# Kernel optimization log

Hardware: AMD Instinct MI355X
Metric: run time of the kernel (lower is better)

The kernel has to match this reference:

```python
import jax, jax.numpy as jnp
import numpy as np

D_MODEL = 1024
NUM_HEADS = 16
DEPTH = D_MODEL // NUM_HEADS
NEG_INF_SCALE = -1e9


def setup_inputs() -> dict:
    key = jax.random.key(0)
    ks = jax.random.split(key, 12)
    B, S = 2, 2048
    q = jax.random.normal(ks[0], (B, S, D_MODEL), dtype=jnp.float32)
    k = jax.random.normal(ks[1], (B, S, D_MODEL), dtype=jnp.float32)
    v = jax.random.normal(ks[2], (B, S, D_MODEL), dtype=jnp.float32)
    # causal mask: 1 where attention is disallowed (future positions)
    mask = jnp.triu(jnp.ones((S, S), dtype=jnp.float32), k=1)[None, None]
    scale = 1.0 / np.sqrt(D_MODEL)
    Wq = jax.random.normal(ks[3], (D_MODEL, D_MODEL), dtype=jnp.float32) * scale
    bq = jnp.zeros((D_MODEL,), dtype=jnp.float32)
    Wk = jax.random.normal(ks[4], (D_MODEL, D_MODEL), dtype=jnp.float32) * scale
    bk = jnp.zeros((D_MODEL,), dtype=jnp.float32)
    Wv = jax.random.normal(ks[5], (D_MODEL, D_MODEL), dtype=jnp.float32) * scale
    bv = jnp.zeros((D_MODEL,), dtype=jnp.float32)
    Wo = jax.random.normal(ks[6], (D_MODEL, D_MODEL), dtype=jnp.float32) * scale
    bo = jnp.zeros((D_MODEL,), dtype=jnp.float32)
    return {"v": v, "k": k, "q": q, "mask": mask,
            "Wq": Wq, "bq": bq, "Wk": Wk, "bk": bk,
            "Wv": Wv, "bv": bv, "Wo": Wo, "bo": bo}


def _split_heads(x):
    B, S, _ = x.shape
    return x.reshape(B, S, NUM_HEADS, DEPTH).transpose(0, 2, 1, 3)  # [B,H,S,depth]


def reference(v, k, q, mask, Wq, bq, Wk, bk, Wv, bv, Wo, bo):
    B, Sq, _ = q.shape
    qh = _split_heads(q @ Wq + bq)  # [B,H,Sq,depth]
    kh = _split_heads(k @ Wk + bk)  # [B,H,Sk,depth]
    vh = _split_heads(v @ Wv + bv)  # [B,H,Sk,depth]
    logits = jnp.einsum('bhqd,bhkd->bhqk', qh, kh) / jnp.sqrt(
        jnp.asarray(DEPTH, dtype=jnp.float32))
    logits = logits + mask * NEG_INF_SCALE
    attn = jax.nn.softmax(logits, axis=-1)
    out = jnp.einsum('bhqk,bhkd->bhqd', attn, vh)  # [B,H,Sq,depth]
    out = out.transpose(0, 2, 1, 3).reshape(B, Sq, D_MODEL)
    return out @ Wo + bo
```

## Files before the change

kernel.cpp:

```cpp
#include <hip/hip_runtime.h>
#include <stdint.h>

#define D_MODEL 1024
#define NHEADS  16
#define DEPTH   64
#define BATCH   2
#define SEQ     2048
#define M_TOT   (BATCH * SEQ)

#define Q_SCALE 0.18033688011112042f

typedef unsigned short u16;
typedef unsigned int   u32;
typedef __attribute__((ext_vector_type(8))) short bf16x8;
typedef __attribute__((ext_vector_type(4))) float f32x4;

__device__ __forceinline__ float bf2f(unsigned int u) {
    union { unsigned int i; float f; } x;
    x.i = (u & 0xffffu) << 16;
    return x.f;
}
__device__ __forceinline__ u16 f2bf(float f) {
    union { float f; unsigned int i; } x;
    x.f = f;
    unsigned int lsb = (x.i >> 16) & 1u;
    x.i += 0x7fffu + lsb;
    return (u16)(x.i >> 16);
}
__device__ __forceinline__ u32 fbits(float f) {
    union { float f; unsigned int i; } x; x.f = f; return x.i;
}
__device__ __forceinline__ float exp2f_hw(float x) {
    return __builtin_amdgcn_exp2f(x);
}

__device__ __forceinline__ int sniff_f32(const u16* q) {
    const int lane = threadIdx.x & 63;
    int cnt = 0;
    #pragma unroll
    for (int j = 0; j < 4; ++j) {
        unsigned int bits = q[2 * (lane + 64 * j)];
        bool susp = ((bits & 0x7fffu) >= 0x4780u);
        cnt += (int)__popcll(__ballot(susp));
    }
    return (cnt >= 32) ? 1 : 0;
}

template <int CTRL>
__device__ __forceinline__ float dppf(float x) {
    int r = __builtin_amdgcn_update_dpp(0, (int)fbits(x), CTRL, 0xF, 0xF, false);
    union { int i; float f; } u; u.i = r; return u.f;
}
__device__ __forceinline__ float redmax16(float x) {
    x = fmaxf(x, dppf<0xB1>(x));
    x = fmaxf(x, dppf<0x4E>(x));
    x = fmaxf(x, dppf<0x124>(x));
    x = fmaxf(x, dppf<0x128>(x));
    return x;
}
__device__ __forceinline__ float redsum16(float x) {
    x += dppf<0xB1>(x);
    x += dppf<0x4E>(x);
    x += dppf<0x124>(x);
    x += dppf<0x128>(x);
    return x;
}

__device__ __forceinline__ void stage16(const u16* g, u16* ldsbase) {
#if __has_builtin(__builtin_amdgcn_global_load_lds)
    __builtin_amdgcn_global_load_lds(
        (const __attribute__((address_space(1))) unsigned int*)g,
        (__attribute__((address_space(3))) unsigned int*)ldsbase, 16, 0, 0);
#else
    int lane = threadIdx.x & 63;
    *(uint4*)(ldsbase + lane * 8) = *(const uint4*)g;
#endif
}

__global__ __launch_bounds__(256)
void prep_kernel(const void* q, const void* k, const void* v,
                 const void* W0, const void* W1, const void* W2, const void* W3,
                 u16* d0, u16* d1, u16* d2,
                 u16* T0, u16* T1, u16* T2, u16* T3) {
    __shared__ u16 t[64][72];
    const int f32 = sniff_f32((const u16*)q);
    const int tid = threadIdx.x;
    const int bid = blockIdx.x;

    if (bid < 6144) {
        const int z = bid / 2048, bx = bid % 2048;
        const void* src = (z == 0) ? q : (z == 1) ? k : v;
        u16* dst = (z == 0) ? d0 : (z == 1) ? d1 : d2;
        const size_t i = ((size_t)bx * 256 + tid) * 8;
        if (f32) {
            const float* s = (const float*)src + i;
            float4 a = *(const float4*)s;
            float4 b = *(const float4*)(s + 4);
            u16 t8[8];
            t8[0] = f2bf(a.x); t8[1] = f2bf(a.y); t8[2] = f2bf(a.z); t8[3] = f2bf(a.w);
            t8[4] = f2bf(b.x); t8[5] = f2bf(b.y); t8[6] = f2bf(b.z); t8[7] = f2bf(b.w);
            *(uint4*)(dst + i) = *(uint4*)t8;
        } else {
            *(uint4*)(dst + i) = *(const uint4*)((const u16*)src + i);
        }
    } else {
        const int r = bid - 6144;
        const int z = r >> 8, rem = r & 255;
        const int n0 = (rem & 15) * 64, k0 = (rem >> 4) * 64;
        const void* Wv = (z == 0) ? W0 : (z == 1) ? W1 : (z == 2) ? W2 : W3;
        u16* WT = (z == 0) ? T0 : (z == 1) ? T1 : (z == 2) ? T2 : T3;

        #pragma unroll
        for (int cb = 0; cb < 2; ++cb) {
            int c = tid + cb * 256;
            int kl = c >> 3, nc = (c & 7) * 8;
            size_t off = (size_t)(k0 + kl) * D_MODEL + n0 + nc;
            u16 tmp[8];
            if (f32) {
                const float* W = (const float*)Wv;
                float4 a = *(const float4*)(W + off);
                float4 b = *(const float4*)(W + off + 4);
                tmp[0] = f2bf(a.x); tmp[1] = f2bf(a.y); tmp[2] = f2bf(a.z); tmp[3] = f2bf(a.w);
                tmp[4] = f2bf(b.x); tmp[5] = f2bf(b.y); tmp[6] = f2bf(b.z); tmp[7] = f2bf(b.w);
            } else {
                *(uint4*)tmp = *(const uint4*)((const u16*)Wv + off);
            }
            *(uint4*)&t[kl][nc] = *(uint4*)tmp;
        }
        __syncthreads();
        #pragma unroll
        for (int cb = 0; cb < 2; ++cb) {
            int c = tid + cb * 256;
            int nl = c >> 3, kc = (c & 7) * 8;
            u16 tmp[8];
            #pragma unroll
            for (int i = 0; i < 8; ++i) tmp[i] = t[kc + i][nl];
            *(uint4*)(WT + (size_t)(n0 + nl) * D_MODEL + k0 + kc) = *(uint4*)tmp;
        }
    }
}

struct GemmJob {
    const u16*  A;
    const u16*  BT;
    const void* bias;
    void*       C;
    int cmode;
    float scale;
};

__global__ __launch_bounds__(256, 4)
void gemm6(GemmJob j0, GemmJob j1, GemmJob j2, const u16* __restrict__ qs) {
    __shared__ u16 Als[2][64 * 64];
    __shared__ u16 Bls[2][64 * 64];

    const u32 lin = blockIdx.x + gridDim.x * (blockIdx.y + gridDim.y * blockIdx.z);
    const u32 xcd = lin & 7, idx = lin >> 3;
    const u32 per = (gridDim.y * gridDim.z) >> 3;
    const u32 mz = xcd * per + (idx >> 3);
    const u32 nb_ = idx & 7;
    const u32 zz = mz / gridDim.y;
    const u32 my2 = mz % gridDim.y;
    const u32 mtile = my2 >> 1, nhalf = my2 & 1;
    GemmJob jb = (zz == 0) ? j0 : (zz == 1) ? j1 : j2;

    const int f32 = sniff_f32(qs);
    const int tid = threadIdx.x;
    const int w = tid >> 6, lane = tid & 63;
    const int cc = lane & 15, quad = lane >> 4;
    const int wm = w >> 1, wn = w & 1;
    const int m0 = mtile * 64, n0 = (nhalf * 8 + nb_) * 64;

    f32x4 zero4 = {0.f, 0.f, 0.f, 0.f};
    f32x4 acc[2][2];
    #pragma unroll
    for (int i = 0; i < 2; ++i)
        #pragma unroll
        for (int j = 0; j < 2; ++j) acc[i][j] = zero4;

    const int srow_off = lane >> 3;
    const int sg8 = ((lane & 7) ^ ((lane >> 3) & 7)) * 8;

    auto stageAB = [&](int buf, int k0) {
        #pragma unroll
        for (int i = 0; i < 2; ++i) {
            int c = w * 2 + i;
            int row = c * 8 + srow_off;
            stage16(jb.BT + (size_t)(n0 + row) * D_MODEL + k0 + sg8, &Bls[buf][c * 512]);
            stage16(jb.A  + (size_t)(m0 + row) * D_MODEL + k0 + sg8, &Als[buf][c * 512]);
        }
    };

    stageAB(0, 0);

    const int NT = D_MODEL / 64;
    for (int t = 0; t < NT; ++t) {
        const int cur = t & 1;
        __syncthreads();
        if (t + 1 < NT) stageAB(cur ^ 1, (t + 1) * 64);

        const int sw = cc & 7;
        bf16x8 af[2][2], bf[2][2];
        #pragma unroll
        for (int i = 0; i < 2; ++i) {
            const u16* ar = &Als[cur][(wm * 32 + i * 16 + cc) * 64];
            af[i][0] = *(const bf16x8*)(ar + ((quad ^ sw) * 8));
            af[i][1] = *(const bf16x8*)(ar + (((4 + quad) ^ sw) * 8));
        }
        #pragma unroll
        for (int j = 0; j < 2; ++j) {
            const u16* br = &Bls[cur][(wn * 32 + j * 16 + cc) * 64];
            bf[j][0] = *(const bf16x8*)(br + ((quad ^ sw) * 8));
            bf[j][1] = *(const bf16x8*)(br + (((4 + quad) ^ sw) * 8));
        }
        __builtin_amdgcn_s_setprio(1);
        #pragma unroll
        for (int i = 0; i < 2; ++i)
            #pragma unroll
            for (int j = 0; j < 2; ++j) {
                acc[i][j] = __builtin_amdgcn_mfma_f32_16x16x32_bf16(af[i][0], bf[j][0], acc[i][j], 0, 0, 0);
                acc[i][j] = __builtin_amdgcn_mfma_f32_16x16x32_bf16(af[i][1], bf[j][1], acc[i][j], 0, 0, 0);
            }
        __builtin_amdgcn_s_setprio(0);
    }

    #pragma unroll
    for (int j = 0; j < 2; ++j) {
        int col = n0 + wn * 32 + j * 16 + cc;
        float bv = f32 ? ((const float*)jb.bias)[col] : bf2f(((const u16*)jb.bias)[col]);
        #pragma unroll
        for (int i = 0; i < 2; ++i)
            #pragma unroll
            for (int r = 0; r < 4; ++r) {
                int row = m0 + wm * 32 + i * 16 + quad * 4 + r;
                float vo = (acc[i][j][r] + bv) * jb.scale;
                if (jb.cmode == 0) {
                    ((u16*)jb.C)[(size_t)row * D_MODEL + col] = f2bf(vo);
                } else if (jb.cmode == 1) {
                    int bb = row >> 11, tok = row & (SEQ - 1);
                    int hh = col >> 6, dd = col & 63;
                    int tile = tok >> 6, n = tok & 63;
                    int kap = ((n & 15) << 2) + (n >> 4);
                    ((u16*)jb.C)[((size_t)((bb * NHEADS + hh) * DEPTH + dd)) * SEQ
                                 + tile * 64 + kap] = f2bf(vo);
                } else {
                    if (f32) ((float*)jb.C)[(size_t)row * D_MODEL + col] = vo;
                    else     ((u16*)jb.C)[(size_t)row * D_MODEL + col] = f2bf(vo);
                }
            }
    }
}

__global__ __launch_bounds__(256, 3)
void attn3(const u16* __restrict__ Qp, const u16* __restrict__ Kp,
           const u16* __restrict__ VpT, u16* __restrict__ Ao) {
    __shared__ u16 Kls[2][64 * 64];
    __shared__ u16 Vls[2][64 * 64];
    __shared__ u16 Pls[4][16][72];

    const int tid = threadIdx.x;
    const int w = tid >> 6, lane = tid & 63;
    const int cc = lane & 15, quad = lane >> 4;

    const u32 lin = blockIdx.x + 32u * (blockIdx.y + 16u * blockIdx.z);
    const int qq = 31 - (int)(lin >> 5);
    const int h  = (int)(lin & 15);
    const int b  = (int)((lin >> 4) & 1);
    const int qbase = qq * 64 + w * 16;

    bf16x8 qf[2];
    {
        const u16* qr = Qp + (size_t)(b * SEQ + qbase + cc) * D_MODEL + h * DEPTH;
        qf[0] = *(const bf16x8*)(qr + quad * 8);
        qf[1] = *(const bf16x8*)(qr + 32 + quad * 8);
    }

    const u16* kbase = Kp + (size_t)(b * SEQ) * D_MODEL + h * DEPTH;
    const u16* vbase = VpT + (size_t)((b * NHEADS + h) * DEPTH) * SEQ;

    const int r8 = lane >> 3;
    const int g8 = ((lane & 7) ^ (r8 & 7)) * 8;

    auto stageKV = [&](int buf, int jt) {
        #pragma unroll
        for (int i = 0; i < 2; ++i) {
            int row = w * 16 + i * 8 + r8;
            stage16(kbase + (size_t)(jt * 64 + row) * D_MODEL + g8,
                    &Kls[buf][(w * 16 + i * 8) * 64]);
            stage16(vbase + (size_t)row * SEQ + jt * 64 + g8,
                    &Vls[buf][(w * 16 + i * 8) * 64]);
        }
    };

    f32x4 zero4 = {0.f, 0.f, 0.f, 0.f};
    f32x4 oacc[4];
    #pragma unroll
    for (int db = 0; db < 4; ++db) oacc[db] = zero4;
    float m_run[4], l_run[4];
    #pragma unroll
    for (int r = 0; r < 4; ++r) { m_run[r] = -1e30f; l_run[r] = 0.f; }

    stageKV(0, 0);

    for (int jt = 0; jt <= qq; ++jt) {
        const int cur = jt & 1;
        __syncthreads();
        if (jt < qq) stageKV(cur ^ 1, jt + 1);

        const int sw = cc & 7;
        bf16x8 kf[4][2];
        #pragma unroll
        for (int nb = 0; nb < 4; ++nb) {
            const u16* kr = &Kls[cur][(nb * 16 + cc) * 64];
            kf[nb][0] = *(const bf16x8*)(kr + ((quad ^ sw) * 8));
            kf[nb][1] = *(const bf16x8*)(kr + (((4 + quad) ^ sw) * 8));
        }
        f32x4 s[4];
        __builtin_amdgcn_s_setprio(1);
        #pragma unroll
        for (int nb = 0; nb < 4; ++nb) {
            s[nb] = __builtin_amdgcn_mfma_f32_16x16x32_bf16(qf[0], kf[nb][0], zero4, 0, 0, 0);
            s[nb] = __builtin_amdgcn_mfma_f32_16x16x32_bf16(qf[1], kf[nb][1], s[nb], 0, 0, 0);
        }
        __builtin_amdgcn_s_setprio(0);

        if (jt == qq) {
            #pragma unroll
            for (int nb = 0; nb < 4; ++nb)
                #pragma unroll
                for (int r = 0; r < 4; ++r)
                    if (nb * 16 + cc > w * 16 + quad * 4 + r) s[nb][r] = -1e30f;
        }

        float alpha[4];
        #pragma unroll
        for (int r = 0; r < 4; ++r) {
            float mrow = redmax16(fmaxf(fmaxf(s[0][r], s[1][r]),
                                        fmaxf(s[2][r], s[3][r])));
            float mn = fmaxf(m_run[r], mrow);
            alpha[r] = exp2f_hw(m_run[r] - mn);
            m_run[r] = mn;
        }
        #pragma unroll
        for (int nb = 0; nb < 4; ++nb)
            #pragma unroll
            for (int r = 0; r < 4; ++r)
                s[nb][r] = exp2f_hw(s[nb][r] - m_run[r]);
        #pragma unroll
        for (int r = 0; r < 4; ++r)
            l_run[r] = l_run[r] * alpha[r]
                     + ((s[0][r] + s[1][r]) + (s[2][r] + s[3][r]));
        #pragma unroll
        for (int db = 0; db < 4; ++db)
            #pragma unroll
            for (int r = 0; r < 4; ++r)
                oacc[db][r] *= alpha[r];

        #pragma unroll
        for (int r = 0; r < 4; ++r) {
            u32 p01 = __builtin_amdgcn_perm(fbits(s[1][r]), fbits(s[0][r]), 0x07060302u);
            u32 p23 = __builtin_amdgcn_perm(fbits(s[3][r]), fbits(s[2][r]), 0x07060302u);
            uint2 pk; pk.x = p01; pk.y = p23;
            *(uint2*)&Pls[w][quad * 4 + r][4 * cc] = pk;
        }
        __asm__ volatile("" ::: "memory");

        bf16x8 pf0 = *(const bf16x8*)&Pls[w][cc][quad * 8];
        bf16x8 pf1 = *(const bf16x8*)&Pls[w][cc][32 + quad * 8];

        __builtin_amdgcn_s_setprio(1);
        #pragma unroll
        for (int db = 0; db < 4; ++db) {
            const u16* vr = &Vls[cur][(db * 16 + cc) * 64];
            bf16x8 v0 = *(const bf16x8*)(vr + ((quad ^ sw) * 8));
            bf16x8 v1 = *(const bf16x8*)(vr + (((4 + quad) ^ sw) * 8));
            oacc[db] = __builtin_amdgcn_mfma_f32_16x16x32_bf16(pf0, v0, oacc[db], 0, 0, 0);
            oacc[db] = __builtin_amdgcn_mfma_f32_16x16x32_bf16(pf1, v1, oacc[db], 0, 0, 0);
        }
        __builtin_amdgcn_s_setprio(0);
    }

    float linv[4];
    #pragma unroll
    for (int r = 0; r < 4; ++r) linv[r] = 1.0f / redsum16(l_run[r]);
    #pragma unroll
    for (int db = 0; db < 4; ++db)
        #pragma unroll
        for (int r = 0; r < 4; ++r) {
            size_t row = (size_t)(b * SEQ + qbase + quad * 4 + r);
            Ao[row * D_MODEL + h * DEPTH + db * 16 + cc] =
                f2bf(oacc[db][r] * linv[r]);
        }
}

extern "C" void kernel_launch(void* const* d_in, const int* in_sizes, int n_in,
                              void* d_out, int out_size, void* d_ws, size_t ws_size,
                              hipStream_t stream) {
    const void* v  = d_in[0];
    const void* k  = d_in[1];
    const void* q  = d_in[2];
    const void* Wq = d_in[4];
    const void* bq = d_in[5];
    const void* Wk = d_in[6];
    const void* bk = d_in[7];
    const void* Wv = d_in[8];
    const void* bv = d_in[9];
    const void* Wo = d_in[10];
    const void* bo = d_in[11];

    char* base = (char*)d_ws;
    const size_t WSZ = (size_t)D_MODEL * D_MODEL;
    const size_t TOK = (size_t)M_TOT * D_MODEL;
    u16* WqT = (u16*)(base + 256);
    u16* WkT = WqT + WSZ;
    u16* WvT = WkT + WSZ;
    u16* WoT = WvT + WSZ;
    u16* Qb  = WoT + WSZ;
    u16* Kb  = Qb + TOK;
    u16* Vb  = Kb + TOK;
    u16* Qp  = Vb + TOK;
    u16* Kp  = Qp + TOK;
    u16* VpT = Kp + TOK;
    u16* Ao  = Qb;

    prep_kernel<<<dim3(7168), 256, 0, stream>>>(q, k, v, Wq, Wk, Wv, Wo,
                                                Qb, Kb, Vb,
                                                WqT, WkT, WvT, WoT);

    GemmJob jq = {Qb, WqT, bq, Qp,    0, Q_SCALE};
    GemmJob jk = {Kb, WkT, bk, Kp,    0, 1.0f};
    GemmJob jv = {Vb, WvT, bv, VpT,   1, 1.0f};
    gemm6<<<dim3(8, 128, 3), 256, 0, stream>>>(jq, jk, jv, (const u16*)q);

    attn3<<<dim3(32, 16, 2), 256, 0, stream>>>(Qp, Kp, VpT, Ao);

    GemmJob jo = {Ao, WoT, bo, d_out, 2, 1.0f};
    gemm6<<<dim3(8, 128, 1), 256, 0, stream>>>(jo, jo, jo, (const u16*)q);
}
```

Before: 244.8 us.

## Fuse fp32-to-bf16 activation conversion into QKV projection GEMM A-tile loads

Drops the separate prep pass that converts q, k and v from fp32 to bf16 buffers. The projection GEMM now loads fp32 A tiles into registers, converts them and writes them to LDS after the MFMAs, while B still uses the direct global-to-LDS path. This removes a full read and write of the activations, but each GEMM block reads twice as many A bytes and does the conversion inside the main loop, which adds register pressure.

```diff
diff --git a/kernel.cpp b/kernel.cpp
--- a/kernel.cpp
+++ b/kernel.cpp
@@ -78,74 +78,54 @@
 }
 
 __global__ __launch_bounds__(256)
-void prep_kernel(const void* q, const void* k, const void* v,
+void prep_kernel(const u16* q,
                  const void* W0, const void* W1, const void* W2, const void* W3,
-                 u16* d0, u16* d1, u16* d2,
                  u16* T0, u16* T1, u16* T2, u16* T3) {
     __shared__ u16 t[64][72];
-    const int f32 = sniff_f32((const u16*)q);
+    const int f32 = sniff_f32(q);
     const int tid = threadIdx.x;
-    const int bid = blockIdx.x;
-
-    if (bid < 6144) {
-        const int z = bid / 2048, bx = bid % 2048;
-        const void* src = (z == 0) ? q : (z == 1) ? k : v;
-        u16* dst = (z == 0) ? d0 : (z == 1) ? d1 : d2;
-        const size_t i = ((size_t)bx * 256 + tid) * 8;
+    const int r = blockIdx.x;
+    const int z = r >> 8, rem = r & 255;
+    const int n0 = (rem & 15) * 64, k0 = (rem >> 4) * 64;
+    const void* Wv = (z == 0) ? W0 : (z == 1) ? W1 : (z == 2) ? W2 : W3;
+    u16* WT = (z == 0) ? T0 : (z == 1) ? T1 : (z == 2) ? T2 : T3;
+
+    #pragma unroll
+    for (int cb = 0; cb < 2; ++cb) {
+        int c = tid + cb * 256;
+        int kl = c >> 3, nc = (c & 7) * 8;
+        size_t off = (size_t)(k0 + kl) * D_MODEL + n0 + nc;
+        u16 tmp[8];
         if (f32) {
-            const float* s = (const float*)src + i;
-            float4 a = *(const float4*)s;
-            float4 b = *(const float4*)(s + 4);
-            u16 t8[8];
-            t8[0] = f2bf(a.x); t8[1] = f2bf(a.y); t8[2] = f2bf(a.z); t8[3] = f2bf(a.w);
-            t8[4] = f2bf(b.x); t8[5] = f2bf(b.y); t8[6] = f2bf(b.z); t8[7] = f2bf(b.w);
-            *(uint4*)(dst + i) = *(uint4*)t8;
+            const float* W = (const float*)Wv;
+            float4 a = *(const float4*)(W + off);
+            float4 b = *(const float4*)(W + off + 4);
+            tmp[0] = f2bf(a.x); tmp[1] = f2bf(a.y); tmp[2] = f2bf(a.z); tmp[3] = f2bf(a.w);
+            tmp[4] = f2bf(b.x); tmp[5] = f2bf(b.y); tmp[6] = f2bf(b.z); tmp[7] = f2bf(b.w);
         } else {
-            *(uint4*)(dst + i) = *(const uint4*)((const u16*)src + i);
-        }
-    } else {
-        const int r = bid - 6144;
-        const int z = r >> 8, rem = r & 255;
-        const int n0 = (rem & 15) * 64, k0 = (rem >> 4) * 64;
-        const void* Wv = (z == 0) ? W0 : (z == 1) ? W1 : (z == 2) ? W2 : W3;
-        u16* WT = (z == 0) ? T0 : (z == 1) ? T1 : (z == 2) ? T2 : T3;
-
-        #pragma unroll
-        for (int cb = 0; cb < 2; ++cb) {
-            int c = tid + cb * 256;
-            int kl = c >> 3, nc = (c & 7) * 8;
-            size_t off = (size_t)(k0 + kl) * D_MODEL + n0 + nc;
-            u16 tmp[8];
-            if (f32) {
-                const float* W = (const float*)Wv;
-                float4 a = *(const float4*)(W + off);
-                float4 b = *(const float4*)(W + off + 4);
-                tmp[0] = f2bf(a.x); tmp[1] = f2bf(a.y); tmp[2] = f2bf(a.z); tmp[3] = f2bf(a.w);
-                tmp[4] = f2bf(b.x); tmp[5] = f2bf(b.y); tmp[6] = f2bf(b.z); tmp[7] = f2bf(b.w);
-            } else {
-                *(uint4*)tmp = *(const uint4*)((const u16*)Wv + off);
-            }
-            *(uint4*)&t[kl][nc] = *(uint4*)tmp;
-        }
-        __syncthreads();
-        #pragma unroll
-        for (int cb = 0; cb < 2; ++cb) {
-            int c = tid + cb * 256;
-            int nl = c >> 3, kc = (c & 7) * 8;
-            u16 tmp[8];
-            #pragma unroll
-            for (int i = 0; i < 8; ++i) tmp[i] = t[kc + i][nl];
-            *(uint4*)(WT + (size_t)(n0 + nl) * D_MODEL + k0 + kc) = *(uint4*)tmp;
-        }
+            *(uint4*)tmp = *(const uint4*)((const u16*)Wv + off);
+        }
+        *(uint4*)&t[kl][nc] = *(uint4*)tmp;
+    }
+    __syncthreads();
+    #pragma unroll
+    for (int cb = 0; cb < 2; ++cb) {
+        int c = tid + cb * 256;
+        int nl = c >> 3, kc = (c & 7) * 8;
+        u16 tmp[8];
+        #pragma unroll
+        for (int i = 0; i < 8; ++i) tmp[i] = t[kc + i][nl];
+        *(uint4*)(WT + (size_t)(n0 + nl) * D_MODEL + k0 + kc) = *(uint4*)tmp;
     }
 }
 
 struct GemmJob {
-    const u16*  A;
+    const void* A;
     const u16*  BT;
     const void* bias;
     void*       C;
     int cmode;
+    int araw;
     float scale;
 };
 
@@ -180,24 +160,62 @@
 
     const int srow_off = lane >> 3;
     const int sg8 = ((lane & 7) ^ ((lane >> 3) & 7)) * 8;
-
-    auto stageAB = [&](int buf, int k0) {
+    const bool acvt = jb.araw && f32;
+
+    auto stageB = [&](int buf, int k0) {
         #pragma unroll
         for (int i = 0; i < 2; ++i) {
             int c = w * 2 + i;
             int row = c * 8 + srow_off;
             stage16(jb.BT + (size_t)(n0 + row) * D_MODEL + k0 + sg8, &Bls[buf][c * 512]);
-            stage16(jb.A  + (size_t)(m0 + row) * D_MODEL + k0 + sg8, &Als[buf][c * 512]);
         }
     };
-
-    stageAB(0, 0);
+    auto stageA_bf = [&](int buf, int k0) {
+        #pragma unroll
+        for (int i = 0; i < 2; ++i) {
+            int c = w * 2 + i;
+            int row = c * 8 + srow_off;
+            stage16((const u16*)jb.A + (size_t)(m0 + row) * D_MODEL + k0 + sg8,
+                    &Als[buf][c * 512]);
+        }
+    };
+    float4 a0v[2], a1v[2];
+    auto aload_f32 = [&](int k0) {
+        #pragma unroll
+        for (int i = 0; i < 2; ++i) {
+            int c = w * 2 + i;
+            int row = c * 8 + srow_off;
+            const float* s = (const float*)jb.A + (size_t)(m0 + row) * D_MODEL + k0 + sg8;
+            a0v[i] = *(const float4*)s;
+            a1v[i] = *(const float4*)(s + 4);
+        }
+    };
+    auto awrite_f32 = [&](int buf) {
+        #pragma unroll
+        for (int i = 0; i < 2; ++i) {
+            int c = w * 2 + i;
+            u16 t8[8];
+            t8[0] = f2bf(a0v[i].x); t8[1] = f2bf(a0v[i].y);
+            t8[2] = f2bf(a0v[i].z); t8[3] = f2bf(a0v[i].w);
+            t8[4] = f2bf(a1v[i].x); t8[5] = f2bf(a1v[i].y);
+            t8[6] = f2bf(a1v[i].z); t8[7] = f2bf(a1v[i].w);
+            *(uint4*)&Als[buf][c * 512 + lane * 8] = *(uint4*)t8;
+        }
+    };
+
+    if (acvt) { aload_f32(0); stageB(0, 0); awrite_f32(0); }
+    else      { stageA_bf(0, 0); stageB(0, 0); }
 
     const int NT = D_MODEL / 64;
     for (int t = 0; t < NT; ++t) {
         const int cur = t & 1;
         __syncthreads();
-        if (t + 1 < NT) stageAB(cur ^ 1, (t + 1) * 64);
+        const bool pf = (t + 1 < NT);
+        if (pf) {
+            stageB(cur ^ 1, (t + 1) * 64);
+            if (acvt) aload_f32((t + 1) * 64);
+            else      stageA_bf(cur ^ 1, (t + 1) * 64);
+        }
 
         const int sw = cc & 7;
         bf16x8 af[2][2], bf[2][2];
@@ -222,6 +240,8 @@
                 acc[i][j] = __builtin_amdgcn_mfma_f32_16x16x32_bf16(af[i][1], bf[j][1], acc[i][j], 0, 0, 0);
             }
         __builtin_amdgcn_s_setprio(0);
+
+        if (pf && acvt) awrite_f32(cur ^ 1);
     }
 
     #pragma unroll
@@ -415,25 +435,21 @@
     u16* WkT = WqT + WSZ;
     u16* WvT = WkT + WSZ;
     u16* WoT = WvT + WSZ;
-    u16* Qb  = WoT + WSZ;
-    u16* Kb  = Qb + TOK;
-    u16* Vb  = Kb + TOK;
-    u16* Qp  = Vb + TOK;
+    u16* Qp  = WoT + WSZ;
     u16* Kp  = Qp + TOK;
     u16* VpT = Kp + TOK;
-    u16* Ao  = Qb;
-
-    prep_kernel<<<dim3(7168), 256, 0, stream>>>(q, k, v, Wq, Wk, Wv, Wo,
-                                                Qb, Kb, Vb,
+    u16* Ao  = VpT + TOK;
+
+    prep_kernel<<<dim3(1024), 256, 0, stream>>>((const u16*)q, Wq, Wk, Wv, Wo,
                                                 WqT, WkT, WvT, WoT);
 
-    GemmJob jq = {Qb, WqT, bq, Qp,    0, Q_SCALE};
-    GemmJob jk = {Kb, WkT, bk, Kp,    0, 1.0f};
-    GemmJob jv = {Vb, WvT, bv, VpT,   1, 1.0f};
+    GemmJob jq = {q, WqT, bq, Qp,    0, 1, Q_SCALE};
+    GemmJob jk = {k, WkT, bk, Kp,    0, 1, 1.0f};
+    GemmJob jv = {v, WvT, bv, VpT,   1, 1, 1.0f};
     gemm6<<<dim3(8, 128, 3), 256, 0, stream>>>(jq, jk, jv, (const u16*)q);
 
     attn3<<<dim3(32, 16, 2), 256, 0, stream>>>(Qp, Kp, VpT, Ao);
 
-    GemmJob jo = {Ao, WoT, bo, d_out, 2, 1.0f};
+    GemmJob jo = {Ao, WoT, bo, d_out, 2, 0, 1.0f};
     gemm6<<<dim3(8, 128, 1), 256, 0, stream>>>(jo, jo, jo, (const u16*)q);
 }
```

Measured after the change: 262.9 us. +7.4%, slower.

## Load GEMM operands directly from global into registers, dropping LDS staging

Applied to the files above, without the earlier changes.

The QKV projection GEMM no longer stages A and B tiles through double-buffered shared memory with barriers. Each lane now loads its MFMA fragments straight from global memory into a register double buffer, prefetching the next K-slice while the current one feeds the MFMAs. This removes LDS traffic and __syncthreads, but gives up sharing of tiles across waves, so each tile row is fetched by two waves and global and L2 traffic roughly doubles. The s_setprio hints are also removed.

```diff
diff --git a/kernel.cpp b/kernel.cpp
--- a/kernel.cpp
+++ b/kernel.cpp
@@ -151,9 +151,6 @@
 
 __global__ __launch_bounds__(256, 4)
 void gemm6(GemmJob j0, GemmJob j1, GemmJob j2, const u16* __restrict__ qs) {
-    __shared__ u16 Als[2][64 * 64];
-    __shared__ u16 Bls[2][64 * 64];
-
     const u32 lin = blockIdx.x + gridDim.x * (blockIdx.y + gridDim.y * blockIdx.z);
     const u32 xcd = lin & 7, idx = lin >> 3;
     const u32 per = (gridDim.y * gridDim.z) >> 3;
@@ -178,50 +175,43 @@
         #pragma unroll
         for (int j = 0; j < 2; ++j) acc[i][j] = zero4;
 
-    const int srow_off = lane >> 3;
-    const int sg8 = ((lane & 7) ^ ((lane >> 3) & 7)) * 8;
-
-    auto stageAB = [&](int buf, int k0) {
-        #pragma unroll
-        for (int i = 0; i < 2; ++i) {
-            int c = w * 2 + i;
-            int row = c * 8 + srow_off;
-            stage16(jb.BT + (size_t)(n0 + row) * D_MODEL + k0 + sg8, &Bls[buf][c * 512]);
-            stage16(jb.A  + (size_t)(m0 + row) * D_MODEL + k0 + sg8, &Als[buf][c * 512]);
-        }
-    };
-
-    stageAB(0, 0);
+    const u16* arow[2], *brow[2];
+    #pragma unroll
+    for (int i = 0; i < 2; ++i) {
+        arow[i] = jb.A  + (size_t)(m0 + wm * 32 + i * 16 + cc) * D_MODEL + quad * 8;
+        brow[i] = jb.BT + (size_t)(n0 + wn * 32 + i * 16 + cc) * D_MODEL + quad * 8;
+    }
 
     const int NT = D_MODEL / 64;
+    bf16x8 afp[2][2][2], bfp[2][2][2];
+
+    #pragma unroll
+    for (int i = 0; i < 2; ++i)
+        #pragma unroll
+        for (int h = 0; h < 2; ++h) {
+            afp[0][i][h] = *(const bf16x8*)(arow[i] + h * 32);
+            bfp[0][i][h] = *(const bf16x8*)(brow[i] + h * 32);
+        }
+
+    #pragma unroll
     for (int t = 0; t < NT; ++t) {
-        const int cur = t & 1;
-        __syncthreads();
-        if (t + 1 < NT) stageAB(cur ^ 1, (t + 1) * 64);
-
-        const int sw = cc & 7;
-        bf16x8 af[2][2], bf[2][2];
-        #pragma unroll
-        for (int i = 0; i < 2; ++i) {
-            const u16* ar = &Als[cur][(wm * 32 + i * 16 + cc) * 64];
-            af[i][0] = *(const bf16x8*)(ar + ((quad ^ sw) * 8));
-            af[i][1] = *(const bf16x8*)(ar + (((4 + quad) ^ sw) * 8));
-        }
-        #pragma unroll
-        for (int j = 0; j < 2; ++j) {
-            const u16* br = &Bls[cur][(wn * 32 + j * 16 + cc) * 64];
-            bf[j][0] = *(const bf16x8*)(br + ((quad ^ sw) * 8));
-            bf[j][1] = *(const bf16x8*)(br + (((4 + quad) ^ sw) * 8));
-        }
-        __builtin_amdgcn_s_setprio(1);
+        const int cs = t & 1, ns = cs ^ 1;
+        if (t + 1 < NT) {
+            #pragma unroll
+            for (int i = 0; i < 2; ++i)
+                #pragma unroll
+                for (int h = 0; h < 2; ++h) {
+                    afp[ns][i][h] = *(const bf16x8*)(arow[i] + (t + 1) * 64 + h * 32);
+                    bfp[ns][i][h] = *(const bf16x8*)(brow[i] + (t + 1) * 64 + h * 32);
+                }
+        }
         #pragma unroll
         for (int i = 0; i < 2; ++i)
             #pragma unroll
             for (int j = 0; j < 2; ++j) {
-                acc[i][j] = __builtin_amdgcn_mfma_f32_16x16x32_bf16(af[i][0], bf[j][0], acc[i][j], 0, 0, 0);
-                acc[i][j] = __builtin_amdgcn_mfma_f32_16x16x32_bf16(af[i][1], bf[j][1], acc[i][j], 0, 0, 0);
+                acc[i][j] = __builtin_amdgcn_mfma_f32_16x16x32_bf16(afp[cs][i][0], bfp[cs][j][0], acc[i][j], 0, 0, 0);
+                acc[i][j] = __builtin_amdgcn_mfma_f32_16x16x32_bf16(afp[cs][i][1], bfp[cs][j][1], acc[i][j], 0, 0, 0);
             }
-        __builtin_amdgcn_s_setprio(0);
     }
 
     #pragma unroll
```

After: 414.5 us. 1.69x slower.
